# Performance work log

Measured on AMD Instinct MI355X. Metric: run time of the kernel, lower is better.

## Reference

```python
import jax, jax.numpy as jnp
import numpy as np

EPS = 1e-12  # F.normalize clamp_min eps


def setup_inputs() -> dict:
    key = jax.random.key(0)
    k1, k2, k3, k4 = jax.random.split(key, 4)
    E, A, D, S = 1000000, 100000, 128, 1024
    return {
        "edge_weights": jax.random.uniform(k1, (E,), dtype=jnp.float32),
        "s_indices": jax.random.randint(k2, (E,), 0, S, dtype=jnp.int32),
        "a_indices": jax.random.randint(k3, (E,), 0, A, dtype=jnp.int32),
        "agent_features": jax.random.normal(k4, (A, D), dtype=jnp.float32),
        "num_s": S,
    }


def reference(edge_weights, s_indices, a_indices, agent_features, num_s):
    # Per-edge gathered agent features: [E, D]
    feats_e = agent_features[a_indices]
    ones = jnp.ones_like(edge_weights)
    counts = jax.ops.segment_sum(ones, s_indices, num_segments=num_s)  # [S]
    safe_counts = jnp.maximum(counts, 1.0)

    # Per-source mean feature: [S, D]
    sum_feats = jax.ops.segment_sum(feats_e, s_indices, num_segments=num_s)
    mean_feats = sum_feats / safe_counts[:, None]

    # L2-normalize (eps-clamped norm, matching F.normalize)
    feats_norm = feats_e / jnp.maximum(
        jnp.linalg.norm(feats_e, axis=1, keepdims=True), EPS)
    mean_norm = mean_feats / jnp.maximum(
        jnp.linalg.norm(mean_feats, axis=1, keepdims=True), EPS)

    # Cosine similarity of each edge's agent features to its source mean: [E]
    sims = jnp.sum(feats_norm * mean_norm[s_indices], axis=1)

    # Per-source mean weight, per-edge variance, similarity-weighted variance
    mean_w = jax.ops.segment_sum(edge_weights, s_indices, num_segments=num_s) / safe_counts
    var = (edge_weights - mean_w[s_indices]) ** 2
    wv = sims * var

    # Per-source mean of weighted variance; sources with <=1 edge contribute 0
    seg_mean_wv = jax.ops.segment_sum(wv, s_indices, num_segments=num_s) / safe_counts
    valid = counts > 1.0
    total = jnp.sum(jnp.where(valid, seg_mean_wv, 0.0))
    return total / num_s
```

## Files before the change

### kernel.cpp

```cpp
#include <hip/hip_runtime.h>
#include <math.h>

#define EPS 1e-12f

static constexpr int S_FIXED = 1024;
static constexpr int D_DIM   = 128;
static constexpr int NBLK    = 512;
static constexpr int P_SPLIT = 4;
static constexpr float INVW  = 1.0f / 32767.0f;

typedef float floatx2 __attribute__((ext_vector_type(2)));

#if defined(__has_builtin)
#if __has_builtin(__builtin_amdgcn_cvt_pk_fp8_f32) && __has_builtin(__builtin_amdgcn_cvt_pk_f32_fp8)
#define USE_HW_FP8 1
#endif
#endif

template <bool HI>
static __device__ __forceinline__ unsigned enc_pair(float a, float b, unsigned old) {
#ifdef USE_HW_FP8
    return (unsigned)__builtin_amdgcn_cvt_pk_fp8_f32(a, b, (int)old, HI);
#else
    auto enc1 = [](float x) -> unsigned {
        unsigned u   = __float_as_uint(x);
        unsigned s   = (u >> 24) & 0x80u;
        unsigned mag = u & 0x7fffffffu;
        unsigned byte;
        if (mag >= 0x3C800000u) {
            unsigned rb = mag + 0x7ffffu + ((mag >> 20) & 1u);
            byte = s | (((rb >> 20) - 960u) & 0x7fu);
        } else {
            float t = __uint_as_float(mag) * 512.0f;
            unsigned m = (unsigned)(int)rintf(t);
            byte = s | m;
        }
        return byte;
    };
    unsigned v = enc1(a) | (enc1(b) << 8);
    return HI ? ((old & 0x0000ffffu) | (v << 16)) : ((old & 0xffff0000u) | v);
#endif
}

template <bool HI>
static __device__ __forceinline__ floatx2 dec_pair(unsigned v) {
#ifdef USE_HW_FP8
    return __builtin_amdgcn_cvt_pk_f32_fp8(v, HI);
#else
    auto dec1 = [](unsigned b) -> float {
        unsigned t = (b & 0x7fu) << 20;
        float a = __uint_as_float(t + 0x3C800000u);
        float r = (t < (1u << 23)) ? (a - 0.015625f) : (0.5f * a);
        return (b & 0x80u) ? -r : r;
    };
    unsigned h = HI ? (v >> 16) : (v & 0xffffu);
    floatx2 o;
    o.x = dec1(h & 0xffu);
    o.y = dec1((h >> 8) & 0xffu);
    return o;
#endif
}

__global__ __launch_bounds__(256) void norm_conv_kernel(const float* __restrict__ feats,
                                                        unsigned char* __restrict__ g8,
                                                        float* __restrict__ r_tab, int A) {
    const int row = blockIdx.x * 16 + (threadIdx.x >> 4);
    const int sl  = threadIdx.x & 15;
    if (row >= A) return;
    const float4* fp = reinterpret_cast<const float4*>(feats + (size_t)row * D_DIM + sl * 8);
    const float4 v0 = fp[0], v1 = fp[1];
    float ss = v0.x*v0.x + v0.y*v0.y + v0.z*v0.z + v0.w*v0.w
             + v1.x*v1.x + v1.y*v1.y + v1.z*v1.z + v1.w*v1.w;
#pragma unroll
    for (int o = 1; o < 16; o <<= 1) ss += __shfl_xor(ss, o);
    const float nrm = sqrtf(ss);
    const float inv = 1.0f / fmaxf(nrm, EPS);
    unsigned lo = enc_pair<false>(v0.x*inv, v0.y*inv, 0u);
    lo = enc_pair<true>(v0.z*inv, v0.w*inv, lo);
    unsigned hi = enc_pair<false>(v1.x*inv, v1.y*inv, 0u);
    hi = enc_pair<true>(v1.z*inv, v1.w*inv, hi);
    *reinterpret_cast<uint2*>(g8 + (size_t)row * D_DIM + sl * 8) = make_uint2(lo, hi);
    if (sl == 0) r_tab[row] = nrm;
}

__global__ __launch_bounds__(256) void hist2_kernel(const int* __restrict__ s_idx,
                                                    int* __restrict__ counts2d,
                                                    int E, int chunk) {
    __shared__ int h[S_FIXED];
    for (int i = threadIdx.x; i < S_FIXED; i += 256) h[i] = 0;
    __syncthreads();
    const int b  = blockIdx.x;
    const int lo = b * chunk;
    const int hi = min(E, lo + chunk);
    for (int i = lo + threadIdx.x; i < hi; i += 256)
        atomicAdd(&h[s_idx[i]], 1);
    __syncthreads();
    for (int i = threadIdx.x; i < S_FIXED; i += 256)
        counts2d[b * S_FIXED + i] = h[i];
}

__global__ __launch_bounds__(256) void scan_blocks_kernel(int* __restrict__ counts2d,
                                                          int* __restrict__ counts) {
    const int wv = threadIdx.x >> 6, lane = threadIdx.x & 63;
    const int s  = blockIdx.x * 4 + wv;
    int running = 0;
    for (int b0 = 0; b0 < NBLK; b0 += 64) {
        const int idx = (b0 + lane) * S_FIXED + s;
        const int c = counts2d[idx];
        int inc = c;
#pragma unroll
        for (int o = 1; o < 64; o <<= 1) {
            int t = __shfl_up(inc, o);
            if (lane >= o) inc += t;
        }
        counts2d[idx] = running + inc - c;
        running += __shfl(inc, 63);
    }
    if (lane == 0) counts[s] = running;
}

__global__ __launch_bounds__(1024) void scan_bins_kernel(const int* __restrict__ counts,
                                                         int* __restrict__ binstart,
                                                         float* __restrict__ out) {
    __shared__ int sh[S_FIXED];
    const int t = threadIdx.x;
    const int c = counts[t];
    sh[t] = c;
    __syncthreads();
    for (int off = 1; off < S_FIXED; off <<= 1) {
        int v = (t >= off) ? sh[t - off] : 0;
        __syncthreads();
        sh[t] += v;
        __syncthreads();
    }
    binstart[t] = sh[t] - c;
    if (t == 0) out[0] = 0.0f;
}

__global__ __launch_bounds__(256) void scatter2_kernel(const int* __restrict__ s_idx,
                                                       const int* __restrict__ a_idx,
                                                       const float* __restrict__ w,
                                                       const int* __restrict__ counts2d,
                                                       const int* __restrict__ binstart,
                                                       unsigned* __restrict__ bin4,
                                                       int E, int chunk) {
    __shared__ int cur[S_FIXED];
    const int b = blockIdx.x;
    for (int i = threadIdx.x; i < S_FIXED; i += 256)
        cur[i] = binstart[i] + counts2d[b * S_FIXED + i];
    __syncthreads();
    const int lo = b * chunk;
    const int hi = min(E, lo + chunk);
    for (int i = lo + threadIdx.x; i < hi; i += 256) {
        const int s   = s_idx[i];
        const int pos = atomicAdd(&cur[s], 1);
        const unsigned w15 = (unsigned)(int)rintf(w[i] * 32767.0f);
        bin4[pos] = (unsigned)a_idx[i] | (w15 << 17);
    }
}

__global__ __launch_bounds__(256) void partial_kernel(
    const unsigned char* __restrict__ g8,
    const float*         __restrict__ r_tab,
    const int*           __restrict__ counts,
    const int*           __restrict__ binstart,
    const unsigned*      __restrict__ bin4,
    float*               __restrict__ part,
    float*               __restrict__ partW,
    int A)
{
    const int s     = blockIdx.x / P_SPLIT;
    const int p     = blockIdx.x % P_SPLIT;
    const int cnt   = counts[s];
    const int start = binstart[s];
    const int end   = start + cnt;
    const int wave  = threadIdx.x >> 6;
    const int lane  = threadIdx.x & 63;
    const int egrp  = lane >> 4;
    const int sl    = lane & 15;

    floatx2 acc[4][4];
#pragma unroll
    for (int v = 0; v < 4; ++v)
#pragma unroll
        for (int q = 0; q < 4; ++q) acc[v][q] = (floatx2)(0.0f);
    float accW = 0.0f;

    auto body = [&](unsigned rec, float mask) {
        int aj = (int)(rec & 0x1FFFFu);
        aj = min(aj, A - 1);
        const float wj = (float)(rec >> 17) * INVW * mask;
        const float rj = r_tab[aj] * mask;
        const uint2 gu = *reinterpret_cast<const uint2*>(g8 + (size_t)aj * D_DIM + sl * 8);
        floatx2 f[4];
        f[0] = dec_pair<false>(gu.x);
        f[1] = dec_pair<true>(gu.x);
        f[2] = dec_pair<false>(gu.y);
        f[3] = dec_pair<true>(gu.y);
        const floatx2 cr  = (floatx2)(rj);
        const floatx2 cu  = (floatx2)(mask);
        const floatx2 cw  = (floatx2)(wj);
        const floatx2 cw2 = (floatx2)(wj * wj);
#pragma unroll
        for (int q = 0; q < 4; ++q) {
            acc[0][q] = __builtin_elementwise_fma(cr,  f[q], acc[0][q]);
            acc[1][q] = __builtin_elementwise_fma(cu,  f[q], acc[1][q]);
            acc[2][q] = __builtin_elementwise_fma(cw,  f[q], acc[2][q]);
            acc[3][q] = __builtin_elementwise_fma(cw2, f[q], acc[3][q]);
        }
    };

    for (int base = start + (p * 4 + wave) * 64; base < end; base += P_SPLIT * 256) {
        const int rem = min(64, end - base);
        if (lane < rem)
            accW += (float)(bin4[base + lane] >> 17) * INVW;

        if (rem == 64) {
#pragma unroll
            for (int j = 0; j < 16; ++j)
                body(bin4[base + 4 * j + egrp], 1.0f);
        } else {
            const int jfull = rem >> 2;
            for (int j = 0; j < jfull; ++j)
                body(bin4[base + 4 * j + egrp], 1.0f);
            if (rem & 3) {
                const int e = (rem & ~3) + egrp;
                body(bin4[base + e], (e < rem) ? 1.0f : 0.0f);
            }
        }
    }

#pragma unroll
    for (int v = 0; v < 4; ++v)
#pragma unroll
        for (int q = 0; q < 4; ++q) {
            acc[v][q].x += __shfl_xor(acc[v][q].x, 16);
            acc[v][q].y += __shfl_xor(acc[v][q].y, 16);
            acc[v][q].x += __shfl_xor(acc[v][q].x, 32);
            acc[v][q].y += __shfl_xor(acc[v][q].y, 32);
        }
#pragma unroll
    for (int o = 32; o > 0; o >>= 1) accW += __shfl_xor(accW, o);

    __shared__ float red[4][4 * D_DIM];
    __shared__ float redW[4];
    if (lane < 16) {
#pragma unroll
        for (int v = 0; v < 4; ++v)
#pragma unroll
            for (int q = 0; q < 4; ++q) {
                red[wave][v * D_DIM + sl * 8 + 2 * q]     = acc[v][q].x;
                red[wave][v * D_DIM + sl * 8 + 2 * q + 1] = acc[v][q].y;
            }
    }
    if (lane == 0) redW[wave] = accW;
    __syncthreads();

    float* po = part + (size_t)(s * P_SPLIT + p) * (4 * D_DIM);
    for (int i = threadIdx.x; i < 4 * D_DIM; i += 256)
        po[i] = red[0][i] + red[1][i] + red[2][i] + red[3][i];
    if (threadIdx.x == 0)
        partW[s * P_SPLIT + p] = redW[0] + redW[1] + redW[2] + redW[3];
}

__global__ __launch_bounds__(1024) void finish_kernel(
    const float* __restrict__ part,
    const float* __restrict__ partW,
    const int*   __restrict__ counts,
    const int*   __restrict__ num_s_ptr,
    float*       __restrict__ out)
{
    const int wv   = threadIdx.x >> 6;
    const int lane = threadIdx.x & 63;
    const int s    = blockIdx.x * 16 + wv;

    float2 V[4];
#pragma unroll
    for (int v = 0; v < 4; ++v) V[v] = make_float2(0.f, 0.f);
    float sumW = 0.0f;
#pragma unroll
    for (int p = 0; p < P_SPLIT; ++p) {
#pragma unroll
        for (int v = 0; v < 4; ++v) {
            const float2 x = *reinterpret_cast<const float2*>(
                part + ((size_t)s * P_SPLIT + p) * (4 * D_DIM) + v * D_DIM + lane * 2);
            V[v].x += x.x; V[v].y += x.y;
        }
        if (lane == 0) sumW += partW[s * P_SPLIT + p];
    }
    const int   cnt      = counts[s];
    const float safe     = (float)max(cnt, 1);
    const float inv_safe = 1.0f / safe;

    const float mx = V[0].x * inv_safe, my = V[0].y * inv_safe;
    float ss = mx * mx + my * my;
    float s0 = V[1].x * mx + V[1].y * my;
    float s1 = V[2].x * mx + V[2].y * my;
    float s2 = V[3].x * mx + V[3].y * my;
#pragma unroll
    for (int o = 32; o > 0; o >>= 1) {
        ss += __shfl_xor(ss, o);
        s0 += __shfl_xor(s0, o);
        s1 += __shfl_xor(s1, o);
        s2 += __shfl_xor(s2, o);
    }

    __shared__ float bl[16];
    if (lane == 0) {
        float contrib = 0.0f;
        if (cnt > 1) {
            const float mw = sumW * inv_safe;
            const float mn = fmaxf(sqrtf(ss), EPS);
            contrib = (s2 - 2.0f * mw * s1 + mw * mw * s0) / mn * inv_safe
                      / (float)(*num_s_ptr);
        }
        bl[wv] = contrib;
    }
    __syncthreads();
    if (threadIdx.x == 0) {
        float t = 0.0f;
#pragma unroll
        for (int i = 0; i < 16; ++i) t += bl[i];
        atomicAdd(out, t);
    }
}

extern "C" void kernel_launch(void* const* d_in, const int* in_sizes, int n_in,
                              void* d_out, int out_size, void* d_ws, size_t ws_size,
                              hipStream_t stream) {
    const float* edge_w  = (const float*)d_in[0];
    const int*   s_idx   = (const int*)d_in[1];
    const int*   a_idx   = (const int*)d_in[2];
    const float* feats   = (const float*)d_in[3];
    const int*   num_s_p = (const int*)d_in[4];

    const int E = in_sizes[0];
    const int A = in_sizes[3] / D_DIM;

    float* out = (float*)d_out;

    char* p = (char*)d_ws;
    unsigned*      bin4     = (unsigned*)p;      p += (size_t)E * 4;
    int*           counts2d = (int*)p;           p += (size_t)NBLK * S_FIXED * 4;
    int*           binstart = (int*)p;           p += S_FIXED * 4;
    int*           counts   = (int*)p;           p += S_FIXED * 4;
    float*         partW    = (float*)p;         p += S_FIXED * P_SPLIT * 4;
    float*         part     = (float*)p;         p += (size_t)S_FIXED * P_SPLIT * 4 * D_DIM * 4;
    float*         r_tab    = (float*)p;         p += (size_t)A * 4;
    unsigned char* g8       = (unsigned char*)p; p += (size_t)A * D_DIM;

    const int chunk = (E + NBLK - 1) / NBLK;

    norm_conv_kernel<<<(A + 15) / 16, 256, 0, stream>>>(feats, g8, r_tab, A);
    hist2_kernel<<<NBLK, 256, 0, stream>>>(s_idx, counts2d, E, chunk);
    scan_blocks_kernel<<<S_FIXED / 4, 256, 0, stream>>>(counts2d, counts);
    scan_bins_kernel<<<1, 1024, 0, stream>>>(counts, binstart, out);
    scatter2_kernel<<<NBLK, 256, 0, stream>>>(s_idx, a_idx, edge_w, counts2d, binstart, bin4, E, chunk);
    partial_kernel<<<S_FIXED * P_SPLIT, 256, 0, stream>>>(g8, r_tab, counts, binstart, bin4, part, partW, A);
    finish_kernel<<<S_FIXED / 16, 1024, 0, stream>>>(part, partW, counts, num_s_p, out);
}
```

Baseline: 87.15 us.

## Fuse norm and histogram launches; batch gathers in partial kernel for memory parallelism

```diff
diff --git a/kernel.cpp b/kernel.cpp
--- a/kernel.cpp
+++ b/kernel.cpp
@@ -61,42 +61,43 @@
 #endif
 }
 
-__global__ __launch_bounds__(256) void norm_conv_kernel(const float* __restrict__ feats,
-                                                        unsigned char* __restrict__ g8,
-                                                        float* __restrict__ r_tab, int A) {
-    const int row = blockIdx.x * 16 + (threadIdx.x >> 4);
-    const int sl  = threadIdx.x & 15;
-    if (row >= A) return;
-    const float4* fp = reinterpret_cast<const float4*>(feats + (size_t)row * D_DIM + sl * 8);
-    const float4 v0 = fp[0], v1 = fp[1];
-    float ss = v0.x*v0.x + v0.y*v0.y + v0.z*v0.z + v0.w*v0.w
-             + v1.x*v1.x + v1.y*v1.y + v1.z*v1.z + v1.w*v1.w;
-#pragma unroll
-    for (int o = 1; o < 16; o <<= 1) ss += __shfl_xor(ss, o);
-    const float nrm = sqrtf(ss);
-    const float inv = 1.0f / fmaxf(nrm, EPS);
-    unsigned lo = enc_pair<false>(v0.x*inv, v0.y*inv, 0u);
-    lo = enc_pair<true>(v0.z*inv, v0.w*inv, lo);
-    unsigned hi = enc_pair<false>(v1.x*inv, v1.y*inv, 0u);
-    hi = enc_pair<true>(v1.z*inv, v1.w*inv, hi);
-    *reinterpret_cast<uint2*>(g8 + (size_t)row * D_DIM + sl * 8) = make_uint2(lo, hi);
-    if (sl == 0) r_tab[row] = nrm;
-}
-
-__global__ __launch_bounds__(256) void hist2_kernel(const int* __restrict__ s_idx,
-                                                    int* __restrict__ counts2d,
-                                                    int E, int chunk) {
-    __shared__ int h[S_FIXED];
-    for (int i = threadIdx.x; i < S_FIXED; i += 256) h[i] = 0;
-    __syncthreads();
-    const int b  = blockIdx.x;
-    const int lo = b * chunk;
-    const int hi = min(E, lo + chunk);
-    for (int i = lo + threadIdx.x; i < hi; i += 256)
-        atomicAdd(&h[s_idx[i]], 1);
-    __syncthreads();
-    for (int i = threadIdx.x; i < S_FIXED; i += 256)
-        counts2d[b * S_FIXED + i] = h[i];
+__global__ __launch_bounds__(256) void normhist_kernel(const float* __restrict__ feats,
+                                                       unsigned char* __restrict__ g8,
+                                                       float* __restrict__ r_tab, int A,
+                                                       const int* __restrict__ s_idx,
+                                                       int* __restrict__ counts2d,
+                                                       int E, int chunk, int ncb) {
+    if (blockIdx.x < (unsigned)ncb) {
+        const int row = blockIdx.x * 16 + (threadIdx.x >> 4);
+        const int sl  = threadIdx.x & 15;
+        if (row >= A) return;
+        const float4* fp = reinterpret_cast<const float4*>(feats + (size_t)row * D_DIM + sl * 8);
+        const float4 v0 = fp[0], v1 = fp[1];
+        float ss = v0.x*v0.x + v0.y*v0.y + v0.z*v0.z + v0.w*v0.w
+                 + v1.x*v1.x + v1.y*v1.y + v1.z*v1.z + v1.w*v1.w;
+#pragma unroll
+        for (int o = 1; o < 16; o <<= 1) ss += __shfl_xor(ss, o);
+        const float nrm = sqrtf(ss);
+        const float inv = 1.0f / fmaxf(nrm, EPS);
+        unsigned lo = enc_pair<false>(v0.x*inv, v0.y*inv, 0u);
+        lo = enc_pair<true>(v0.z*inv, v0.w*inv, lo);
+        unsigned hi = enc_pair<false>(v1.x*inv, v1.y*inv, 0u);
+        hi = enc_pair<true>(v1.z*inv, v1.w*inv, hi);
+        *reinterpret_cast<uint2*>(g8 + (size_t)row * D_DIM + sl * 8) = make_uint2(lo, hi);
+        if (sl == 0) r_tab[row] = nrm;
+    } else {
+        __shared__ int h[S_FIXED];
+        for (int i = threadIdx.x; i < S_FIXED; i += 256) h[i] = 0;
+        __syncthreads();
+        const int b  = blockIdx.x - ncb;
+        const int lo = b * chunk;
+        const int hi = min(E, lo + chunk);
+        for (int i = lo + threadIdx.x; i < hi; i += 256)
+            atomicAdd(&h[s_idx[i]], 1);
+        __syncthreads();
+        for (int i = threadIdx.x; i < S_FIXED; i += 256)
+            counts2d[b * S_FIXED + i] = h[i];
+    }
 }
 
 __global__ __launch_bounds__(256) void scan_blocks_kernel(int* __restrict__ counts2d,
@@ -159,7 +160,7 @@
     }
 }
 
-__global__ __launch_bounds__(256) void partial_kernel(
+__global__ __launch_bounds__(256, 4) void partial_kernel(
     const unsigned char* __restrict__ g8,
     const float*         __restrict__ r_tab,
     const int*           __restrict__ counts,
@@ -186,46 +187,45 @@
         for (int q = 0; q < 4; ++q) acc[v][q] = (floatx2)(0.0f);
     float accW = 0.0f;
 
-    auto body = [&](unsigned rec, float mask) {
-        int aj = (int)(rec & 0x1FFFFu);
-        aj = min(aj, A - 1);
-        const float wj = (float)(rec >> 17) * INVW * mask;
-        const float rj = r_tab[aj] * mask;
-        const uint2 gu = *reinterpret_cast<const uint2*>(g8 + (size_t)aj * D_DIM + sl * 8);
-        floatx2 f[4];
-        f[0] = dec_pair<false>(gu.x);
-        f[1] = dec_pair<true>(gu.x);
-        f[2] = dec_pair<false>(gu.y);
-        f[3] = dec_pair<true>(gu.y);
-        const floatx2 cr  = (floatx2)(rj);
-        const floatx2 cu  = (floatx2)(mask);
-        const floatx2 cw  = (floatx2)(wj);
-        const floatx2 cw2 = (floatx2)(wj * wj);
-#pragma unroll
-        for (int q = 0; q < 4; ++q) {
-            acc[0][q] = __builtin_elementwise_fma(cr,  f[q], acc[0][q]);
-            acc[1][q] = __builtin_elementwise_fma(cu,  f[q], acc[1][q]);
-            acc[2][q] = __builtin_elementwise_fma(cw,  f[q], acc[2][q]);
-            acc[3][q] = __builtin_elementwise_fma(cw2, f[q], acc[3][q]);
-        }
-    };
-
     for (int base = start + (p * 4 + wave) * 64; base < end; base += P_SPLIT * 256) {
         const int rem = min(64, end - base);
         if (lane < rem)
             accW += (float)(bin4[base + lane] >> 17) * INVW;
 
-        if (rem == 64) {
-#pragma unroll
-            for (int j = 0; j < 16; ++j)
-                body(bin4[base + 4 * j + egrp], 1.0f);
-        } else {
-            const int jfull = rem >> 2;
-            for (int j = 0; j < jfull; ++j)
-                body(bin4[base + 4 * j + egrp], 1.0f);
-            if (rem & 3) {
-                const int e = (rem & ~3) + egrp;
-                body(bin4[base + e], (e < rem) ? 1.0f : 0.0f);
+        unsigned recs[16];
+#pragma unroll
+        for (int j = 0; j < 16; ++j)
+            recs[j] = bin4[base + 4 * j + egrp];
+
+        uint2 gu[16];
+        float rj[16];
+#pragma unroll
+        for (int j = 0; j < 16; ++j) {
+            const int aj = min((int)(recs[j] & 0x1FFFFu), A - 1);
+            gu[j] = *reinterpret_cast<const uint2*>(g8 + (size_t)aj * D_DIM + sl * 8);
+            rj[j] = r_tab[aj];
+        }
+
+#pragma unroll
+        for (int j = 0; j < 16; ++j) {
+            const int   e    = 4 * j + egrp;
+            const float mask = (e < rem) ? 1.0f : 0.0f;
+            const float wj   = (float)(recs[j] >> 17) * INVW * mask;
+            floatx2 f[4];
+            f[0] = dec_pair<false>(gu[j].x);
+            f[1] = dec_pair<true>(gu[j].x);
+            f[2] = dec_pair<false>(gu[j].y);
+            f[3] = dec_pair<true>(gu[j].y);
+            const floatx2 cr  = (floatx2)(rj[j] * mask);
+            const floatx2 cu  = (floatx2)(mask);
+            const floatx2 cw  = (floatx2)(wj);
+            const floatx2 cw2 = (floatx2)(wj * wj);
+#pragma unroll
+            for (int q = 0; q < 4; ++q) {
+                acc[0][q] = __builtin_elementwise_fma(cr,  f[q], acc[0][q]);
+                acc[1][q] = __builtin_elementwise_fma(cu,  f[q], acc[1][q]);
+                acc[2][q] = __builtin_elementwise_fma(cw,  f[q], acc[2][q]);
+                acc[3][q] = __builtin_elementwise_fma(cw2, f[q], acc[3][q]);
             }
         }
     }
@@ -350,9 +350,10 @@
     unsigned char* g8       = (unsigned char*)p; p += (size_t)A * D_DIM;
 
     const int chunk = (E + NBLK - 1) / NBLK;
-
-    norm_conv_kernel<<<(A + 15) / 16, 256, 0, stream>>>(feats, g8, r_tab, A);
-    hist2_kernel<<<NBLK, 256, 0, stream>>>(s_idx, counts2d, E, chunk);
+    const int ncb   = (A + 15) / 16;
+
+    normhist_kernel<<<ncb + NBLK, 256, 0, stream>>>(feats, g8, r_tab, A,
+                                                    s_idx, counts2d, E, chunk, ncb);
     scan_blocks_kernel<<<S_FIXED / 4, 256, 0, stream>>>(counts2d, counts);
     scan_bins_kernel<<<1, 1024, 0, stream>>>(counts, binstart, out);
     scatter2_kernel<<<NBLK, 256, 0, stream>>>(s_idx, a_idx, edge_w, counts2d, binstart, bin4, E, chunk);
```

After: 107.2 us. 23.0% more time.

## Bin edges by source and agent range, map ranges to XCDs, fuse norm with histogram

Applied to the files above, without the earlier changes.

```diff
diff --git a/kernel.cpp b/kernel.cpp
--- a/kernel.cpp
+++ b/kernel.cpp
@@ -5,8 +5,10 @@
 
 static constexpr int S_FIXED = 1024;
 static constexpr int D_DIM   = 128;
-static constexpr int NBLK    = 512;
-static constexpr int P_SPLIT = 4;
+static constexpr int NBLK    = 256;
+static constexpr int ARSHIFT = 15;
+static constexpr int NRANGE  = 4;
+static constexpr int NBIN    = S_FIXED * NRANGE;
 static constexpr float INVW  = 1.0f / 32767.0f;
 
 typedef float floatx2 __attribute__((ext_vector_type(2)));
@@ -61,51 +63,56 @@
 #endif
 }
 
-__global__ __launch_bounds__(256) void norm_conv_kernel(const float* __restrict__ feats,
-                                                        unsigned char* __restrict__ g8,
-                                                        float* __restrict__ r_tab, int A) {
-    const int row = blockIdx.x * 16 + (threadIdx.x >> 4);
-    const int sl  = threadIdx.x & 15;
-    if (row >= A) return;
-    const float4* fp = reinterpret_cast<const float4*>(feats + (size_t)row * D_DIM + sl * 8);
-    const float4 v0 = fp[0], v1 = fp[1];
-    float ss = v0.x*v0.x + v0.y*v0.y + v0.z*v0.z + v0.w*v0.w
-             + v1.x*v1.x + v1.y*v1.y + v1.z*v1.z + v1.w*v1.w;
-#pragma unroll
-    for (int o = 1; o < 16; o <<= 1) ss += __shfl_xor(ss, o);
-    const float nrm = sqrtf(ss);
-    const float inv = 1.0f / fmaxf(nrm, EPS);
-    unsigned lo = enc_pair<false>(v0.x*inv, v0.y*inv, 0u);
-    lo = enc_pair<true>(v0.z*inv, v0.w*inv, lo);
-    unsigned hi = enc_pair<false>(v1.x*inv, v1.y*inv, 0u);
-    hi = enc_pair<true>(v1.z*inv, v1.w*inv, hi);
-    *reinterpret_cast<uint2*>(g8 + (size_t)row * D_DIM + sl * 8) = make_uint2(lo, hi);
-    if (sl == 0) r_tab[row] = nrm;
-}
-
-__global__ __launch_bounds__(256) void hist2_kernel(const int* __restrict__ s_idx,
-                                                    int* __restrict__ counts2d,
-                                                    int E, int chunk) {
-    __shared__ int h[S_FIXED];
-    for (int i = threadIdx.x; i < S_FIXED; i += 256) h[i] = 0;
-    __syncthreads();
-    const int b  = blockIdx.x;
-    const int lo = b * chunk;
-    const int hi = min(E, lo + chunk);
-    for (int i = lo + threadIdx.x; i < hi; i += 256)
-        atomicAdd(&h[s_idx[i]], 1);
-    __syncthreads();
-    for (int i = threadIdx.x; i < S_FIXED; i += 256)
-        counts2d[b * S_FIXED + i] = h[i];
+__global__ __launch_bounds__(256) void normhist_kernel(const float* __restrict__ feats,
+                                                       unsigned char* __restrict__ g8,
+                                                       float* __restrict__ r_tab, int A,
+                                                       const int* __restrict__ s_idx,
+                                                       const int* __restrict__ a_idx,
+                                                       int* __restrict__ counts2d,
+                                                       int E, int chunk, int ncb) {
+    if (blockIdx.x < (unsigned)ncb) {
+        const int row = blockIdx.x * 16 + (threadIdx.x >> 4);
+        const int sl  = threadIdx.x & 15;
+        if (row >= A) return;
+        const float4* fp = reinterpret_cast<const float4*>(feats + (size_t)row * D_DIM + sl * 8);
+        const float4 v0 = fp[0], v1 = fp[1];
+        float ss = v0.x*v0.x + v0.y*v0.y + v0.z*v0.z + v0.w*v0.w
+                 + v1.x*v1.x + v1.y*v1.y + v1.z*v1.z + v1.w*v1.w;
+#pragma unroll
+        for (int o = 1; o < 16; o <<= 1) ss += __shfl_xor(ss, o);
+        const float nrm = sqrtf(ss);
+        const float inv = 1.0f / fmaxf(nrm, EPS);
+        unsigned lo = enc_pair<false>(v0.x*inv, v0.y*inv, 0u);
+        lo = enc_pair<true>(v0.z*inv, v0.w*inv, lo);
+        unsigned hi = enc_pair<false>(v1.x*inv, v1.y*inv, 0u);
+        hi = enc_pair<true>(v1.z*inv, v1.w*inv, hi);
+        *reinterpret_cast<uint2*>(g8 + (size_t)row * D_DIM + sl * 8) = make_uint2(lo, hi);
+        if (sl == 0) r_tab[row] = nrm;
+    } else {
+        __shared__ int h[NBIN];
+        for (int i = threadIdx.x; i < NBIN; i += 256) h[i] = 0;
+        __syncthreads();
+        const int b  = blockIdx.x - ncb;
+        const int lo = b * chunk;
+        const int hi = min(E, lo + chunk);
+        for (int i = lo + threadIdx.x; i < hi; i += 256) {
+            const int key = s_idx[i] | ((a_idx[i] >> ARSHIFT) << 10);
+            atomicAdd(&h[key], 1);
+        }
+        __syncthreads();
+        for (int i = threadIdx.x; i < NBIN; i += 256)
+            counts2d[b * NBIN + i] = h[i];
+    }
 }
 
 __global__ __launch_bounds__(256) void scan_blocks_kernel(int* __restrict__ counts2d,
                                                           int* __restrict__ counts) {
     const int wv = threadIdx.x >> 6, lane = threadIdx.x & 63;
-    const int s  = blockIdx.x * 4 + wv;
+    const int bin = blockIdx.x * 4 + wv;
     int running = 0;
+#pragma unroll
     for (int b0 = 0; b0 < NBLK; b0 += 64) {
-        const int idx = (b0 + lane) * S_FIXED + s;
+        const int idx = (b0 + lane) * NBIN + bin;
         const int c = counts2d[idx];
         int inc = c;
 #pragma unroll
@@ -116,24 +123,28 @@
         counts2d[idx] = running + inc - c;
         running += __shfl(inc, 63);
     }
-    if (lane == 0) counts[s] = running;
+    if (lane == 0) counts[bin] = running;
 }
 
 __global__ __launch_bounds__(1024) void scan_bins_kernel(const int* __restrict__ counts,
                                                          int* __restrict__ binstart,
                                                          float* __restrict__ out) {
-    __shared__ int sh[S_FIXED];
+    __shared__ int sh[1024];
     const int t = threadIdx.x;
-    const int c = counts[t];
-    sh[t] = c;
+    int c[4]; int sum = 0;
+#pragma unroll
+    for (int i = 0; i < 4; ++i) { c[i] = counts[t * 4 + i]; sum += c[i]; }
+    sh[t] = sum;
     __syncthreads();
-    for (int off = 1; off < S_FIXED; off <<= 1) {
+    for (int off = 1; off < 1024; off <<= 1) {
         int v = (t >= off) ? sh[t - off] : 0;
         __syncthreads();
         sh[t] += v;
         __syncthreads();
     }
-    binstart[t] = sh[t] - c;
+    int base = sh[t] - sum;
+#pragma unroll
+    for (int i = 0; i < 4; ++i) { binstart[t * 4 + i] = base; base += c[i]; }
     if (t == 0) out[0] = 0.0f;
 }
 
@@ -144,18 +155,19 @@
                                                        const int* __restrict__ binstart,
                                                        unsigned* __restrict__ bin4,
                                                        int E, int chunk) {
-    __shared__ int cur[S_FIXED];
+    __shared__ int cur[NBIN];
     const int b = blockIdx.x;
-    for (int i = threadIdx.x; i < S_FIXED; i += 256)
-        cur[i] = binstart[i] + counts2d[b * S_FIXED + i];
+    for (int i = threadIdx.x; i < NBIN; i += 256)
+        cur[i] = binstart[i] + counts2d[b * NBIN + i];
     __syncthreads();
     const int lo = b * chunk;
     const int hi = min(E, lo + chunk);
     for (int i = lo + threadIdx.x; i < hi; i += 256) {
-        const int s   = s_idx[i];
-        const int pos = atomicAdd(&cur[s], 1);
+        const int a   = a_idx[i];
+        const int key = s_idx[i] | ((a >> ARSHIFT) << 10);
+        const int pos = atomicAdd(&cur[key], 1);
         const unsigned w15 = (unsigned)(int)rintf(w[i] * 32767.0f);
-        bin4[pos] = (unsigned)a_idx[i] | (w15 << 17);
+        bin4[pos] = (unsigned)a | (w15 << 17);
     }
 }
 
@@ -169,10 +181,14 @@
     float*               __restrict__ partW,
     int A)
 {
-    const int s     = blockIdx.x / P_SPLIT;
-    const int p     = blockIdx.x % P_SPLIT;
-    const int cnt   = counts[s];
-    const int start = binstart[s];
+    const int b      = blockIdx.x;
+    const int xcd    = b & 7;
+    const int arange = xcd >> 1;
+    const int s      = ((b >> 3) << 1) | (xcd & 1);
+    const int bi     = (arange << 10) | s;
+
+    const int cnt   = counts[bi];
+    const int start = binstart[bi];
     const int end   = start + cnt;
     const int wave  = threadIdx.x >> 6;
     const int lane  = threadIdx.x & 63;
@@ -210,7 +226,7 @@
         }
     };
 
-    for (int base = start + (p * 4 + wave) * 64; base < end; base += P_SPLIT * 256) {
+    for (int base = start + wave * 64; base < end; base += 256) {
         const int rem = min(64, end - base);
         if (lane < rem)
             accW += (float)(bin4[base + lane] >> 17) * INVW;
@@ -256,11 +272,11 @@
     if (lane == 0) redW[wave] = accW;
     __syncthreads();
 
-    float* po = part + (size_t)(s * P_SPLIT + p) * (4 * D_DIM);
+    float* po = part + (size_t)bi * (4 * D_DIM);
     for (int i = threadIdx.x; i < 4 * D_DIM; i += 256)
         po[i] = red[0][i] + red[1][i] + red[2][i] + red[3][i];
     if (threadIdx.x == 0)
-        partW[s * P_SPLIT + p] = redW[0] + redW[1] + redW[2] + redW[3];
+        partW[bi] = redW[0] + redW[1] + redW[2] + redW[3];
 }
 
 __global__ __launch_bounds__(1024) void finish_kernel(
@@ -278,17 +294,19 @@
 #pragma unroll
     for (int v = 0; v < 4; ++v) V[v] = make_float2(0.f, 0.f);
     float sumW = 0.0f;
-#pragma unroll
-    for (int p = 0; p < P_SPLIT; ++p) {
+    int   cnt  = 0;
+#pragma unroll
+    for (int ar = 0; ar < NRANGE; ++ar) {
+        const int bi = (ar << 10) | s;
 #pragma unroll
         for (int v = 0; v < 4; ++v) {
             const float2 x = *reinterpret_cast<const float2*>(
-                part + ((size_t)s * P_SPLIT + p) * (4 * D_DIM) + v * D_DIM + lane * 2);
+                part + (size_t)bi * (4 * D_DIM) + v * D_DIM + lane * 2);
             V[v].x += x.x; V[v].y += x.y;
         }
-        if (lane == 0) sumW += partW[s * P_SPLIT + p];
-    }
-    const int   cnt      = counts[s];
+        if (lane == 0) sumW += partW[bi];
+        cnt += counts[bi];
+    }
     const float safe     = (float)max(cnt, 1);
     const float inv_safe = 1.0f / safe;
 
@@ -341,21 +359,22 @@
 
     char* p = (char*)d_ws;
     unsigned*      bin4     = (unsigned*)p;      p += (size_t)E * 4;
-    int*           counts2d = (int*)p;           p += (size_t)NBLK * S_FIXED * 4;
-    int*           binstart = (int*)p;           p += S_FIXED * 4;
-    int*           counts   = (int*)p;           p += S_FIXED * 4;
-    float*         partW    = (float*)p;         p += S_FIXED * P_SPLIT * 4;
-    float*         part     = (float*)p;         p += (size_t)S_FIXED * P_SPLIT * 4 * D_DIM * 4;
+    int*           counts2d = (int*)p;           p += (size_t)NBLK * NBIN * 4;
+    int*           binstart = (int*)p;           p += NBIN * 4;
+    int*           counts   = (int*)p;           p += NBIN * 4;
+    float*         partW    = (float*)p;         p += NBIN * 4;
+    float*         part     = (float*)p;         p += (size_t)NBIN * 4 * D_DIM * 4;
     float*         r_tab    = (float*)p;         p += (size_t)A * 4;
     unsigned char* g8       = (unsigned char*)p; p += (size_t)A * D_DIM;
 
     const int chunk = (E + NBLK - 1) / NBLK;
-
-    norm_conv_kernel<<<(A + 15) / 16, 256, 0, stream>>>(feats, g8, r_tab, A);
-    hist2_kernel<<<NBLK, 256, 0, stream>>>(s_idx, counts2d, E, chunk);
-    scan_blocks_kernel<<<S_FIXED / 4, 256, 0, stream>>>(counts2d, counts);
+    const int ncb   = (A + 15) / 16;
+
+    normhist_kernel<<<ncb + NBLK, 256, 0, stream>>>(feats, g8, r_tab, A,
+                                                    s_idx, a_idx, counts2d, E, chunk, ncb);
+    scan_blocks_kernel<<<NBIN / 4, 256, 0, stream>>>(counts2d, counts);
     scan_bins_kernel<<<1, 1024, 0, stream>>>(counts, binstart, out);
     scatter2_kernel<<<NBLK, 256, 0, stream>>>(s_idx, a_idx, edge_w, counts2d, binstart, bin4, E, chunk);
-    partial_kernel<<<S_FIXED * P_SPLIT, 256, 0, stream>>>(g8, r_tab, counts, binstart, bin4, part, partW, A);
+    partial_kernel<<<NBIN, 256, 0, stream>>>(g8, r_tab, counts, binstart, bin4, part, partW, A);
     finish_kernel<<<S_FIXED / 16, 1024, 0, stream>>>(part, partW, counts, num_s_p, out);
 }
```

Result: slower. 105.3 us (+20.8%).
